# Optimization experiments

Measured on AMD Instinct MI355X. Metric: run time of the kernel, lower is better.

Reference implementation:

```python
import jax, jax.numpy as jnp
import numpy as np

B, S, D = 4, 4096, 256


def setup_inputs() -> dict:
    key = jax.random.key(0)
    ks = jax.random.split(key, 8)
    inv = 1.0 / np.sqrt(D)
    return {
        "input_tensor": jax.random.normal(ks[0], (B, S, D), dtype=jnp.float32),
        "attention_mask": jax.random.randint(ks[1], (B, S, S), 0, 2) == 1,
        "Wq": jax.random.uniform(ks[2], (D, D), jnp.float32, -inv, inv),
        "bq": jax.random.uniform(ks[3], (D,), jnp.float32, -inv, inv),
        "Wk": jax.random.uniform(ks[4], (D, D), jnp.float32, -inv, inv),
        "bk": jax.random.uniform(ks[5], (D,), jnp.float32, -inv, inv),
        "Wv": jax.random.uniform(ks[6], (D, D), jnp.float32, -inv, inv),
        "bv": jax.random.uniform(ks[7], (D,), jnp.float32, -inv, inv),
    }


def reference(input_tensor, attention_mask, Wq, bq, Wk, bk, Wv, bv):
    # Linear projections: y = x @ W.T + b  (nn.Linear convention, W is [out,in])
    query = jnp.einsum("bsd,ed->bse", input_tensor, Wq) + bq
    key = jnp.einsum("bsd,ed->bse", input_tensor, Wk) + bk
    value = jnp.einsum("bsd,ed->bse", input_tensor, Wv) + bv
    # Faithful quirk: original scales by sqrt(query.size(1)) == sqrt(seq_len)
    scale = jnp.asarray(query.shape[1], query.dtype) ** 0.5
    scores = jnp.einsum("bqd,bkd->bqk", query, key) / scale  # [B,S,S]
    scores = jnp.where(attention_mask, jnp.asarray(-1e9, scores.dtype), scores)
    attn = jax.nn.softmax(scores, axis=-1)
    # dropout with p=0.0 is identity (eval-mode reference)
    context = jnp.einsum("bqk,bkd->bqd", attn, value)
    return context
```

## Files before the change

### kernel.cpp

```cpp
#include <hip/hip_runtime.h>
#include <hip/hip_bf16.h>
#include <stdint.h>

#define BB 4
#define SS 4096
#define DD 256

typedef __attribute__((ext_vector_type(4))) float f32x4;
typedef __attribute__((ext_vector_type(8))) short s16x8;

__device__ __forceinline__ ushort f2bf(float f) {
  __hip_bfloat16 h = __float2bfloat16(f);
  return __builtin_bit_cast(ushort, h);
}

__device__ __forceinline__ s16x8 pack8(const float* __restrict__ p) {
  const float4 a = *(const float4*)p;
  const float4 b = *(const float4*)(p + 4);
  s16x8 r;
  r[0] = (short)f2bf(a.x); r[1] = (short)f2bf(a.y);
  r[2] = (short)f2bf(a.z); r[3] = (short)f2bf(a.w);
  r[4] = (short)f2bf(b.x); r[5] = (short)f2bf(b.y);
  r[6] = (short)f2bf(b.z); r[7] = (short)f2bf(b.w);
  return r;
}

#define LROW 40

__global__ __launch_bounds__(256) void proj_gemm(const float* __restrict__ X,
                                                 const float* __restrict__ Wq,
                                                 const float* __restrict__ Wk,
                                                 const float* __restrict__ Wv,
                                                 const float* __restrict__ bq,
                                                 const float* __restrict__ bk,
                                                 const float* __restrict__ bv,
                                                 ushort* __restrict__ Qb,
                                                 ushort* __restrict__ Kb,
                                                 ushort* __restrict__ Vt) {
  __shared__ ushort Al[128 * LROW];
  __shared__ ushort Bl[128 * LROW];
  const int m0 = blockIdx.x * 128;
  const int n0 = blockIdx.y * 128;
  const int region = n0 >> 8;
  const int n0l = n0 & 255;
  const float* Wsel = (region == 0) ? Wq : (region == 1) ? Wk : Wv;
  const float* bsel = (region == 0) ? bq : (region == 1) ? bk : bv;
  const int t = threadIdx.x;
  const int lane = t & 63;
  const int w = t >> 6;
  const int wr = w & 1, wc = w >> 1;
  const int col = lane & 15;
  const int quad = lane >> 4;

  f32x4 acc[4][4];
#pragma unroll
  for (int i = 0; i < 4; i++)
#pragma unroll
    for (int j = 0; j < 4; j++) acc[i][j] = f32x4{0.f, 0.f, 0.f, 0.f};

  const int ci0 = t, ci1 = 256 + t;
  const int r0 = ci0 >> 2, c0 = ci0 & 3;
  const int r1 = ci1 >> 2, c1 = ci1 & 3;

  s16x8 pa0 = pack8(X + (size_t)(m0 + r0) * DD + c0 * 8);
  s16x8 pa1 = pack8(X + (size_t)(m0 + r1) * DD + c1 * 8);
  s16x8 pb0 = pack8(Wsel + (size_t)(n0l + r0) * DD + c0 * 8);
  s16x8 pb1 = pack8(Wsel + (size_t)(n0l + r1) * DD + c1 * 8);

  for (int kk = 0; kk < DD; kk += 32) {
    __syncthreads();
    *(s16x8*)&Al[r0 * LROW + c0 * 8] = pa0;
    *(s16x8*)&Al[r1 * LROW + c1 * 8] = pa1;
    *(s16x8*)&Bl[r0 * LROW + c0 * 8] = pb0;
    *(s16x8*)&Bl[r1 * LROW + c1 * 8] = pb1;
    __syncthreads();
    const int kn = kk + 32;
    if (kn < DD) {
      pa0 = pack8(X + (size_t)(m0 + r0) * DD + kn + c0 * 8);
      pa1 = pack8(X + (size_t)(m0 + r1) * DD + kn + c1 * 8);
      pb0 = pack8(Wsel + (size_t)(n0l + r0) * DD + kn + c0 * 8);
      pb1 = pack8(Wsel + (size_t)(n0l + r1) * DD + kn + c1 * 8);
    }
    s16x8 af[4], bfr[4];
#pragma unroll
    for (int mi = 0; mi < 4; mi++)
      af[mi] = *(const s16x8*)&Al[(wr * 64 + mi * 16 + col) * LROW + quad * 8];
#pragma unroll
    for (int ni = 0; ni < 4; ni++)
      bfr[ni] = *(const s16x8*)&Bl[(wc * 64 + ni * 16 + col) * LROW + quad * 8];
#pragma unroll
    for (int mi = 0; mi < 4; mi++)
#pragma unroll
      for (int ni = 0; ni < 4; ni++)
        acc[mi][ni] = __builtin_amdgcn_mfma_f32_16x16x32_bf16(af[mi], bfr[ni], acc[mi][ni], 0, 0, 0);
  }

#pragma unroll
  for (int mi = 0; mi < 4; mi++) {
    const int gm = m0 + wr * 64 + mi * 16 + quad * 4;
#pragma unroll
    for (int ni = 0; ni < 4; ni++) {
      const int gnl = n0l + wc * 64 + ni * 16 + col;
      const float bb = bsel[gnl];
      f32x4 v = acc[mi][ni];
      if (region == 0) {
#pragma unroll
        for (int rg = 0; rg < 4; rg++)
          Qb[(size_t)(gm + rg) * DD + gnl] = f2bf((v[rg] + bb) * 0.015625f);
      } else if (region == 1) {
#pragma unroll
        for (int rg = 0; rg < 4; rg++)
          Kb[(size_t)(gm + rg) * DD + gnl] = f2bf(v[rg] + bb);
      } else {
        const int b = gm >> 12;
        const int s = gm & (SS - 1);
        ushort4 o = { f2bf(v[0] + bb), f2bf(v[1] + bb), f2bf(v[2] + bb), f2bf(v[3] + bb) };
        *(ushort4*)&Vt[((size_t)(b << 8) + gnl) * SS + s] = o;
      }
    }
  }
}

#define NKT 32
#define KROW 264
#define VROW 32
#define PROW 32

#define KVREG_U 8448
#define PL_U (16 * PROW)
#define POFF (2 * KVREG_U)
#define SM_U (POFF + 8 * PL_U)

#define XSTRIDE 72

__global__ __launch_bounds__(512) void attn_kernel(const ushort* __restrict__ Qb,
                                                   const ushort* __restrict__ Kb,
                                                   const ushort* __restrict__ Vt,
                                                   const int* __restrict__ mask,
                                                   float* __restrict__ out,
                                                   float* __restrict__ O1,
                                                   float* __restrict__ Ml) {
  __shared__ __align__(16) ushort sm[SM_U];

  const int qt = blockIdx.x;
  const int b = blockIdx.y;
  const int z = blockIdx.z;
  const int t = threadIdx.x;
  const int g = t >> 8;
  const int tg = t & 255;
  const int lane = t & 63;
  const int w = tg >> 6;
  const int w8 = t >> 6;
  const int col = lane & 15;
  const int quad = lane >> 4;

  ushort* Kl = sm + g * KVREG_U;
  ushort* Vl = sm + g * KVREG_U;
  ushort* Pw = sm + POFF + w8 * PL_U;

  const int q0 = qt * 64;
  const int qrow = q0 + w * 16;

  s16x8 qf[8];
  {
    const ushort* qp = Qb + ((size_t)b * SS + qrow + col) * DD + quad * 8;
#pragma unroll
    for (int dc = 0; dc < 8; dc++) qf[dc] = *(const s16x8*)(qp + dc * 32);
  }

  int kr[4], kc[4], vd[4], vc[4];
#pragma unroll
  for (int i = 0; i < 4; i++) {
    const int ci = i * 256 + tg;
    kr[i] = ci >> 5; kc[i] = ci & 31;
    vd[i] = ci >> 2; vc[i] = ci & 3;
  }

  const ushort* Kg = Kb + (size_t)b * SS * DD;
  const ushort* Vg = Vt + (size_t)b * DD * SS;
  const int* Mg = mask + ((size_t)b * SS + qrow + quad * 4) * SS;

  f32x4 Oc[16];
#pragma unroll
  for (int i = 0; i < 16; i++) Oc[i] = f32x4{0.f, 0.f, 0.f, 0.f};
  float m_i[4] = {-INFINITY, -INFINITY, -INFINITY, -INFINITY};
  float l_i[4] = {0.f, 0.f, 0.f, 0.f};

  const int NT2 = 1024 / NKT;
  const int kb0 = z * 2048 + g * 1024;

  s16x8 pk[4], pv[4];
  int pm[2][4];
#pragma unroll
  for (int i = 0; i < 4; i++) {
    pk[i] = *(const s16x8*)(Kg + (size_t)(kb0 + kr[i]) * DD + kc[i] * 8);
    pv[i] = *(const s16x8*)(Vg + (size_t)vd[i] * SS + kb0 + vc[i] * 8);
  }
#pragma unroll
  for (int jt = 0; jt < 2; jt++)
#pragma unroll
    for (int rg = 0; rg < 4; rg++) pm[jt][rg] = Mg[rg * SS + kb0 + jt * 16 + col];

  for (int tt = 0; tt < NT2; tt++) {
    __syncthreads();
#pragma unroll
    for (int i = 0; i < 4; i++)
      *(s16x8*)&Kl[kr[i] * KROW + kc[i] * 8] = pk[i];
    __syncthreads();
    int mcur[2][4];
#pragma unroll
    for (int jt = 0; jt < 2; jt++)
#pragma unroll
      for (int rg = 0; rg < 4; rg++) mcur[jt][rg] = pm[jt][rg];
    const int k0n = kb0 + (tt + 1) * NKT;
    if (tt + 1 < NT2) {
#pragma unroll
      for (int i = 0; i < 4; i++)
        pk[i] = *(const s16x8*)(Kg + ((size_t)k0n + kr[i]) * DD + kc[i] * 8);
#pragma unroll
      for (int jt = 0; jt < 2; jt++)
#pragma unroll
        for (int rg = 0; rg < 4; rg++) pm[jt][rg] = Mg[rg * SS + k0n + jt * 16 + col];
    }

    f32x4 st[2];
    __builtin_amdgcn_s_setprio(1);
#pragma unroll
    for (int jt = 0; jt < 2; jt++) {
      f32x4 s = f32x4{0.f, 0.f, 0.f, 0.f};
#pragma unroll
      for (int dc = 0; dc < 8; dc++) {
        s16x8 kb = *(const s16x8*)&Kl[(jt * 16 + col) * KROW + dc * 32 + quad * 8];
        s = __builtin_amdgcn_mfma_f32_16x16x32_bf16(qf[dc], kb, s, 0, 0, 0);
      }
      st[jt] = s;
    }
    __builtin_amdgcn_s_setprio(0);
#pragma unroll
    for (int jt = 0; jt < 2; jt++)
#pragma unroll
      for (int rg = 0; rg < 4; rg++)
        if (mcur[jt][rg]) st[jt][rg] = -1e9f;

    float al[4];
#pragma unroll
    for (int rg = 0; rg < 4; rg++) {
      float v = fmaxf(st[0][rg], st[1][rg]);
      v = fmaxf(v, __shfl_xor(v, 1));
      v = fmaxf(v, __shfl_xor(v, 2));
      v = fmaxf(v, __shfl_xor(v, 4));
      v = fmaxf(v, __shfl_xor(v, 8));
      const float mn = fmaxf(m_i[rg], v);
      al[rg] = __expf(m_i[rg] - mn);
      m_i[rg] = mn;
    }
#pragma unroll
    for (int rg = 0; rg < 4; rg++) {
      const float p0 = __expf(st[0][rg] - m_i[rg]);
      const float p1 = __expf(st[1][rg] - m_i[rg]);
      st[0][rg] = p0; st[1][rg] = p1;
      float s2 = p0 + p1;
      s2 += __shfl_xor(s2, 1);
      s2 += __shfl_xor(s2, 2);
      s2 += __shfl_xor(s2, 4);
      s2 += __shfl_xor(s2, 8);
      l_i[rg] = l_i[rg] * al[rg] + s2;
    }

#pragma unroll
    for (int jt = 0; jt < 2; jt++)
#pragma unroll
      for (int rg = 0; rg < 4; rg++)
        Pw[(quad * 4 + rg) * PROW + jt * 16 + col] = f2bf(st[jt][rg]);
    s16x8 pa = *(const s16x8*)&Pw[col * PROW + quad * 8];

    {
      const bool need = (al[0] < 1.f) | (al[1] < 1.f) | (al[2] < 1.f) | (al[3] < 1.f);
      if (__any(need)) {
#pragma unroll
        for (int dt = 0; dt < 16; dt++)
#pragma unroll
          for (int rg = 0; rg < 4; rg++) Oc[dt][rg] *= al[rg];
      }
    }

    __syncthreads();
#pragma unroll
    for (int i = 0; i < 4; i++)
      *(s16x8*)&Vl[vd[i] * VROW + vc[i] * 8] = pv[i];
    if (tt + 1 < NT2) {
#pragma unroll
      for (int i = 0; i < 4; i++)
        pv[i] = *(const s16x8*)(Vg + (size_t)vd[i] * SS + k0n + vc[i] * 8);
    }
    __syncthreads();

    __builtin_amdgcn_s_setprio(1);
#pragma unroll
    for (int dt = 0; dt < 16; dt++) {
      s16x8 vb = *(const s16x8*)&Vl[(dt * 16 + col) * VROW + quad * 8];
      Oc[dt] = __builtin_amdgcn_mfma_f32_16x16x32_bf16(pa, vb, Oc[dt], 0, 0, 0);
    }
    __builtin_amdgcn_s_setprio(0);
  }

  float* ex = (float*)sm;
#pragma unroll
  for (int rr = 0; rr < 2; rr++) {
    __syncthreads();
    if (g == 1 && (w >> 1) == rr) {
      float* slot = ex + (size_t)((w & 1) * 64 + lane) * XSTRIDE;
#pragma unroll
      for (int rg = 0; rg < 4; rg++) { slot[rg] = m_i[rg]; slot[4 + rg] = l_i[rg]; }
#pragma unroll
      for (int dt = 0; dt < 16; dt++) *(f32x4*)&slot[8 + dt * 4] = Oc[dt];
    }
    __syncthreads();
    if (g == 0 && (w >> 1) == rr) {
      const float* slot = ex + (size_t)((w & 1) * 64 + lane) * XSTRIDE;
      float a0[4], a1[4];
#pragma unroll
      for (int rg = 0; rg < 4; rg++) {
        const float m1 = slot[rg];
        const float l1 = slot[4 + rg];
        const float mm = fmaxf(m_i[rg], m1);
        a0[rg] = __expf(m_i[rg] - mm);
        a1[rg] = __expf(m1 - mm);
        m_i[rg] = mm;
        l_i[rg] = l_i[rg] * a0[rg] + l1 * a1[rg];
      }
#pragma unroll
      for (int dt = 0; dt < 16; dt++) {
        const f32x4 o1 = *(const f32x4*)&slot[8 + dt * 4];
#pragma unroll
        for (int rg = 0; rg < 4; rg++)
          Oc[dt][rg] = Oc[dt][rg] * a0[rg] + o1[rg] * a1[rg];
      }
    }
  }
  if (g == 0) {
    float* op = (z ? O1 : out) + ((size_t)b * SS + qrow + quad * 4) * DD;
#pragma unroll
    for (int dt = 0; dt < 16; dt++) {
#pragma unroll
      for (int rg = 0; rg < 4; rg++)
        op[rg * DD + dt * 16 + col] = Oc[dt][rg];
    }
    if (col == 0) {
      float2* pml = (float2*)Ml + (size_t)z * BB * SS + (size_t)b * SS + qrow + quad * 4;
#pragma unroll
      for (int rg = 0; rg < 4; rg++) pml[rg] = make_float2(m_i[rg], l_i[rg]);
    }
  }
}

__global__ __launch_bounds__(256) void merge_kernel(const float* __restrict__ Ml,
                                                    const float* __restrict__ O1,
                                                    float* __restrict__ out) {
  const int row = blockIdx.x * 4 + (threadIdx.x >> 6);
  const int lane = threadIdx.x & 63;
  const float2 ml0 = ((const float2*)Ml)[row];
  const float2 ml1 = ((const float2*)Ml)[BB * SS + row];
  const float mm = fmaxf(ml0.x, ml1.x);
  const float a0 = __expf(ml0.x - mm);
  const float a1 = __expf(ml1.x - mm);
  const float inv = 1.0f / (ml0.y * a0 + ml1.y * a1);
  f32x4* po = (f32x4*)out + (size_t)row * 64 + lane;
  const f32x4 o0 = *po;
  const f32x4 o1 = ((const f32x4*)O1)[(size_t)row * 64 + lane];
  f32x4 r;
#pragma unroll
  for (int j = 0; j < 4; j++) r[j] = (o0[j] * a0 + o1[j] * a1) * inv;
  *po = r;
}

extern "C" void kernel_launch(void* const* d_in, const int* in_sizes, int n_in,
                              void* d_out, int out_size, void* d_ws, size_t ws_size,
                              hipStream_t stream) {
  const float* X  = (const float*)d_in[0];
  const int* mask = (const int*)d_in[1];
  const float* Wq = (const float*)d_in[2];
  const float* bq = (const float*)d_in[3];
  const float* Wk = (const float*)d_in[4];
  const float* bk = (const float*)d_in[5];
  const float* Wv = (const float*)d_in[6];
  const float* bv = (const float*)d_in[7];
  float* out = (float*)d_out;

  ushort* base = (ushort*)d_ws;
  ushort* Qb = base;
  ushort* Kb = Qb + (size_t)BB * SS * DD;
  ushort* Vt = Kb + (size_t)BB * SS * DD;
  float* O1 = (float*)(Vt + (size_t)BB * SS * DD);
  float* Ml = O1 + (size_t)BB * SS * DD;

  proj_gemm<<<dim3(128, 6), 256, 0, stream>>>(X, Wq, Wk, Wv, bq, bk, bv, Qb, Kb, Vt);
  attn_kernel<<<dim3(64, 4, 2), 512, 0, stream>>>(Qb, Kb, Vt, mask, out, O1, Ml);
  merge_kernel<<<(BB * SS) / 4, 256, 0, stream>>>(Ml, O1, out);
}
```

Measured before the change: 521.0 us.

## Replace in-block KV split with 256-thread blocks and wider grid split-K

The 512-thread attention block, which split the key range between two 256-thread groups and merged them through shared memory, becomes a 256-thread block with a 4-block occupancy hint. The key-range split moves into the grid, with up to four z-splits depending on workspace size, and the merge kernel now combines a variable number of partial outputs. Shared-memory row strides for V and P are padded from 32 to 40 to reduce bank conflicts. This removes the in-block shared-memory merge and its barriers and aims for better occupancy. In exchange, more partial outputs are written to and reread from global memory.

```diff
diff --git a/kernel.cpp b/kernel.cpp
--- a/kernel.cpp
+++ b/kernel.cpp
@@ -123,43 +123,38 @@
 
 #define NKT 32
 #define KROW 264
-#define VROW 32
-#define PROW 32
-
-#define KVREG_U 8448
+#define VROW 40
+#define PROW 40
+
+#define KVREG_U 10240
 #define PL_U (16 * PROW)
-#define POFF (2 * KVREG_U)
-#define SM_U (POFF + 8 * PL_U)
-
-#define XSTRIDE 72
-
-__global__ __launch_bounds__(512) void attn_kernel(const ushort* __restrict__ Qb,
-                                                   const ushort* __restrict__ Kb,
-                                                   const ushort* __restrict__ Vt,
-                                                   const int* __restrict__ mask,
-                                                   float* __restrict__ out,
-                                                   float* __restrict__ O1,
-                                                   float* __restrict__ Ml) {
+#define POFF KVREG_U
+#define SM_U (POFF + 4 * PL_U)
+
+__global__ __launch_bounds__(256, 4) void attn_kernel(const ushort* __restrict__ Qb,
+                                                      const ushort* __restrict__ Kb,
+                                                      const ushort* __restrict__ Vt,
+                                                      const int* __restrict__ mask,
+                                                      float* __restrict__ out,
+                                                      float* __restrict__ Opart,
+                                                      float* __restrict__ Ml,
+                                                      const int NT2) {
   __shared__ __align__(16) ushort sm[SM_U];
 
   const int qt = blockIdx.x;
   const int b = blockIdx.y;
   const int z = blockIdx.z;
   const int t = threadIdx.x;
-  const int g = t >> 8;
-  const int tg = t & 255;
   const int lane = t & 63;
-  const int w = tg >> 6;
-  const int w8 = t >> 6;
+  const int w = t >> 6;
   const int col = lane & 15;
   const int quad = lane >> 4;
 
-  ushort* Kl = sm + g * KVREG_U;
-  ushort* Vl = sm + g * KVREG_U;
-  ushort* Pw = sm + POFF + w8 * PL_U;
-
-  const int q0 = qt * 64;
-  const int qrow = q0 + w * 16;
+  ushort* Kl = sm;
+  ushort* Vl = sm;
+  ushort* Pw = sm + POFF + w * PL_U;
+
+  const int qrow = qt * 64 + w * 16;
 
   s16x8 qf[8];
   {
@@ -171,7 +166,7 @@
   int kr[4], kc[4], vd[4], vc[4];
 #pragma unroll
   for (int i = 0; i < 4; i++) {
-    const int ci = i * 256 + tg;
+    const int ci = i * 256 + t;
     kr[i] = ci >> 5; kc[i] = ci & 31;
     vd[i] = ci >> 2; vc[i] = ci & 3;
   }
@@ -186,8 +181,7 @@
   float m_i[4] = {-INFINITY, -INFINITY, -INFINITY, -INFINITY};
   float l_i[4] = {0.f, 0.f, 0.f, 0.f};
 
-  const int NT2 = 1024 / NKT;
-  const int kb0 = z * 2048 + g * 1024;
+  const int kb0 = z * NT2 * NKT;
 
   s16x8 pk[4], pv[4];
   int pm[2][4];
@@ -304,74 +298,52 @@
     __builtin_amdgcn_s_setprio(0);
   }
 
-  float* ex = (float*)sm;
-#pragma unroll
-  for (int rr = 0; rr < 2; rr++) {
-    __syncthreads();
-    if (g == 1 && (w >> 1) == rr) {
-      float* slot = ex + (size_t)((w & 1) * 64 + lane) * XSTRIDE;
-#pragma unroll
-      for (int rg = 0; rg < 4; rg++) { slot[rg] = m_i[rg]; slot[4 + rg] = l_i[rg]; }
-#pragma unroll
-      for (int dt = 0; dt < 16; dt++) *(f32x4*)&slot[8 + dt * 4] = Oc[dt];
-    }
-    __syncthreads();
-    if (g == 0 && (w >> 1) == rr) {
-      const float* slot = ex + (size_t)((w & 1) * 64 + lane) * XSTRIDE;
-      float a0[4], a1[4];
-#pragma unroll
-      for (int rg = 0; rg < 4; rg++) {
-        const float m1 = slot[rg];
-        const float l1 = slot[4 + rg];
-        const float mm = fmaxf(m_i[rg], m1);
-        a0[rg] = __expf(m_i[rg] - mm);
-        a1[rg] = __expf(m1 - mm);
-        m_i[rg] = mm;
-        l_i[rg] = l_i[rg] * a0[rg] + l1 * a1[rg];
-      }
-#pragma unroll
-      for (int dt = 0; dt < 16; dt++) {
-        const f32x4 o1 = *(const f32x4*)&slot[8 + dt * 4];
-#pragma unroll
-        for (int rg = 0; rg < 4; rg++)
-          Oc[dt][rg] = Oc[dt][rg] * a0[rg] + o1[rg] * a1[rg];
-      }
-    }
-  }
-  if (g == 0) {
-    float* op = (z ? O1 : out) + ((size_t)b * SS + qrow + quad * 4) * DD;
-#pragma unroll
-    for (int dt = 0; dt < 16; dt++) {
-#pragma unroll
-      for (int rg = 0; rg < 4; rg++)
-        op[rg * DD + dt * 16 + col] = Oc[dt][rg];
-    }
-    if (col == 0) {
-      float2* pml = (float2*)Ml + (size_t)z * BB * SS + (size_t)b * SS + qrow + quad * 4;
-#pragma unroll
-      for (int rg = 0; rg < 4; rg++) pml[rg] = make_float2(m_i[rg], l_i[rg]);
-    }
+  float* op = (z == 0 ? out : Opart + (size_t)(z - 1) * BB * SS * DD) +
+              ((size_t)b * SS + qrow + quad * 4) * DD;
+#pragma unroll
+  for (int dt = 0; dt < 16; dt++) {
+#pragma unroll
+    for (int rg = 0; rg < 4; rg++)
+      op[rg * DD + dt * 16 + col] = Oc[dt][rg];
+  }
+  if (col == 0) {
+    float2* pml = (float2*)Ml + (size_t)z * BB * SS + (size_t)b * SS + qrow + quad * 4;
+#pragma unroll
+    for (int rg = 0; rg < 4; rg++) pml[rg] = make_float2(m_i[rg], l_i[rg]);
   }
 }
 
 __global__ __launch_bounds__(256) void merge_kernel(const float* __restrict__ Ml,
-                                                    const float* __restrict__ O1,
-                                                    float* __restrict__ out) {
+                                                    const float* __restrict__ Opart,
+                                                    float* __restrict__ out,
+                                                    const int nz) {
   const int row = blockIdx.x * 4 + (threadIdx.x >> 6);
   const int lane = threadIdx.x & 63;
-  const float2 ml0 = ((const float2*)Ml)[row];
-  const float2 ml1 = ((const float2*)Ml)[BB * SS + row];
-  const float mm = fmaxf(ml0.x, ml1.x);
-  const float a0 = __expf(ml0.x - mm);
-  const float a1 = __expf(ml1.x - mm);
-  const float inv = 1.0f / (ml0.y * a0 + ml1.y * a1);
+  float mz[4], lz[4];
+  float mm = -INFINITY;
+  for (int zz = 0; zz < nz; zz++) {
+    const float2 ml = ((const float2*)Ml)[(size_t)zz * BB * SS + row];
+    mz[zz] = ml.x; lz[zz] = ml.y;
+    mm = fmaxf(mm, ml.x);
+  }
+  float a[4], L = 0.f;
+  for (int zz = 0; zz < nz; zz++) {
+    a[zz] = __expf(mz[zz] - mm);
+    L += lz[zz] * a[zz];
+  }
+  const float inv = 1.0f / L;
   f32x4* po = (f32x4*)out + (size_t)row * 64 + lane;
-  const f32x4 o0 = *po;
-  const f32x4 o1 = ((const f32x4*)O1)[(size_t)row * 64 + lane];
-  f32x4 r;
-#pragma unroll
-  for (int j = 0; j < 4; j++) r[j] = (o0[j] * a0 + o1[j] * a1) * inv;
-  *po = r;
+  f32x4 acc = *po;
+#pragma unroll 4
+  for (int j = 0; j < 4; j++) acc[j] *= a[0];
+  for (int zz = 1; zz < nz; zz++) {
+    const f32x4 o = ((const f32x4*)(Opart + (size_t)(zz - 1) * BB * SS * DD))[(size_t)row * 64 + lane];
+#pragma unroll 4
+    for (int j = 0; j < 4; j++) acc[j] += o[j] * a[zz];
+  }
+#pragma unroll 4
+  for (int j = 0; j < 4; j++) acc[j] *= inv;
+  *po = acc;
 }
 
 extern "C" void kernel_launch(void* const* d_in, const int* in_sizes, int n_in,
@@ -391,10 +363,15 @@
   ushort* Qb = base;
   ushort* Kb = Qb + (size_t)BB * SS * DD;
   ushort* Vt = Kb + (size_t)BB * SS * DD;
-  float* O1 = (float*)(Vt + (size_t)BB * SS * DD);
-  float* Ml = O1 + (size_t)BB * SS * DD;
+  float* Ml = (float*)(Vt + (size_t)BB * SS * DD);
+  float* Opart = Ml + (size_t)8 * BB * SS;
+
+  const size_t fixed = (size_t)3 * BB * SS * DD * 2 + (size_t)8 * BB * SS * 4;
+  const size_t need4 = fixed + (size_t)3 * BB * SS * DD * 4;
+  const int nz = (ws_size >= need4) ? 4 : 2;
+  const int NT2 = (SS / NKT) / nz;
 
   proj_gemm<<<dim3(128, 6), 256, 0, stream>>>(X, Wq, Wk, Wv, bq, bk, bv, Qb, Kb, Vt);
-  attn_kernel<<<dim3(64, 4, 2), 512, 0, stream>>>(Qb, Kb, Vt, mask, out, O1, Ml);
-  merge_kernel<<<(BB * SS) / 4, 256, 0, stream>>>(Ml, O1, out);
-}
+  attn_kernel<<<dim3(64, 4, nz), 256, 0, stream>>>(Qb, Kb, Vt, mask, out, Opart, Ml, NT2);
+  merge_kernel<<<(BB * SS) / 4, 256, 0, stream>>>(Ml, Opart, out, nz);
+}
```

New measurement: 1.156 ms. 2.22x slower.
